# Optimization experiments

Hardware: AMD Instinct MI355X
Metric: run time of the kernel (lower is better)

Reference implementation:

```python
import jax, jax.numpy as jnp
import numpy as np


def setup_inputs() -> dict:
    key = jax.random.key(0)
    ks = jax.random.split(key, 10)
    N, CZ, CH = 512, 128, 128
    s = 1.0 / np.sqrt(CZ)  # keep pre-sigmoid activations in a sane range
    return {
        "z": jax.random.normal(ks[0], (N, N, CZ), dtype=jnp.float32),
        "mask": jnp.ones((N, N, 1), dtype=jnp.float32),
        "weight_ag": jax.random.normal(ks[1], (CH, CZ), dtype=jnp.float32) * s,
        "bias_ag": jax.random.normal(ks[2], (CH,), dtype=jnp.float32) * 0.02,
        "weight_ap": jax.random.normal(ks[3], (CH, CZ), dtype=jnp.float32) * s,
        "bias_ap": jax.random.normal(ks[4], (CH,), dtype=jnp.float32) * 0.02,
        "weight_bg": jax.random.normal(ks[5], (CH, CZ), dtype=jnp.float32) * s,
        "bias_bg": jax.random.normal(ks[6], (CH,), dtype=jnp.float32) * 0.02,
        "weight_bp": jax.random.normal(ks[7], (CH, CZ), dtype=jnp.float32) * s,
        "bias_bp": jax.random.normal(ks[8], (CH,), dtype=jnp.float32) * 0.02,
        "chunk_size": 32,
    }


def _triangle_mul(z, mask, w_ag, b_ag, w_ap, b_ap, w_bg, b_bg, w_bp, b_bp):
    # z: [N, N, c_z]; mask: [N, N, 1]; weights: [c, c_z]
    # a = mask * sigmoid(Linear_ag(z)) * Linear_ap(z)   -> [N, N, c]
    a = mask * jax.nn.sigmoid(jnp.einsum("ijz,cz->ijc", z, w_ag) + b_ag) * (
        jnp.einsum("ijz,cz->ijc", z, w_ap) + b_ap
    )
    b = mask * jax.nn.sigmoid(jnp.einsum("ijz,cz->ijc", z, w_bg) + b_bg) * (
        jnp.einsum("ijz,cz->ijc", z, w_bp) + b_bp
    )
    # outgoing triangle multiplicative combination, channel-first output [c, N, N]
    return jnp.einsum("ikc,jkc->cij", a, b)


def reference(z, mask, weight_ag, bias_ag, weight_ap, bias_ap,
              weight_bg, bias_bg, weight_bp, bias_bp, chunk_size):
    # The torch wrapper chunks the hidden-channel dim of the weights and
    # concatenates the per-chunk [c, N, N] outputs along dim 0. Since every
    # channel is independent, this is mathematically identical to running the
    # full computation at once; we do that (clean, fused form).
    return _triangle_mul(z, mask, weight_ag, bias_ag, weight_ap, bias_ap,
                         weight_bg, bias_bg, weight_bp, bias_bp)
```

## Files before the change

### kernel.cpp

```cpp
#include <hip/hip_runtime.h>
#include <stdint.h>


#define NDIM 512
#define CZ   128
#define CH   128
#define NPOS (NDIM * NDIM)

typedef __attribute__((ext_vector_type(8))) __bf16 bf16x8;
typedef __attribute__((ext_vector_type(4))) float  f32x4;

__device__ __forceinline__ unsigned short f2bf(float f) {
  unsigned int u = __builtin_bit_cast(unsigned int, f);
  unsigned int r = (u + 0x7fffu + ((u >> 16) & 1u)) >> 16;
  return (unsigned short)r;
}
__device__ __forceinline__ float bf2f_lo(unsigned int u) {
  return __builtin_bit_cast(float, u << 16);
}
__device__ __forceinline__ float bf2f_hi(unsigned int u) {
  return __builtin_bit_cast(float, u & 0xffff0000u);
}

__global__ __launch_bounds__(256) void conv_weights(
    const float* __restrict__ wag, const float* __restrict__ wap,
    const float* __restrict__ wbg, const float* __restrict__ wbp,
    unsigned short* __restrict__ wbf) {
  int idx = blockIdx.x * 256 + threadIdx.x;
  int proj = idx >> 14;
  int rem  = idx & 16383;
  const float* src = (proj == 0) ? wag : (proj == 1) ? wap : (proj == 2) ? wbg : wbp;
  wbf[idx] = f2bf(src[rem]);
}

__global__ __launch_bounds__(256, 3) void proj_fuse(
    const float* __restrict__ z,
    const float* __restrict__ mask,
    const unsigned short* __restrict__ wbf,
    const float* __restrict__ bias_ag, const float* __restrict__ bias_ap,
    const float* __restrict__ bias_bg, const float* __restrict__ bias_bp,
    unsigned short* __restrict__ a_ws,
    unsigned short* __restrict__ b_ws) {
  __shared__ unsigned short zbuf[32 * 136];
  __shared__ unsigned short accb[4 * 128 * 36];

  const int t    = threadIdx.x;
  const int lane = t & 63;
  const int w    = t >> 6;
  const int m0   = blockIdx.x * 32;

  {
    const int c4 = t & 31;
    const int rb = t >> 5;
#pragma unroll
    for (int it = 0; it < 4; ++it) {
      const int row = it * 8 + rb;
      const float4 v = *(const float4*)(z + (size_t)(m0 + row) * CZ + c4 * 4);
      unsigned int lo = (unsigned int)f2bf(v.x) | ((unsigned int)f2bf(v.y) << 16);
      unsigned int hi = (unsigned int)f2bf(v.z) | ((unsigned int)f2bf(v.w) << 16);
      *(uint2*)&zbuf[row * 136 + c4 * 4] = make_uint2(lo, hi);
    }
  }
  __syncthreads();

  const int ml    = lane & 15;
  const int q     = lane >> 4;
  const int koffl = q * 8;

  f32x4 acc[2][8];
#pragma unroll
  for (int mi = 0; mi < 2; ++mi)
#pragma unroll
    for (int ni = 0; ni < 8; ++ni) acc[mi][ni] = (f32x4){0.f, 0.f, 0.f, 0.f};

#pragma unroll
  for (int ks = 0; ks < 4; ++ks) {
    bf16x8 af0 = *(const bf16x8*)&zbuf[(ml)      * 136 + ks * 32 + koffl];
    bf16x8 af1 = *(const bf16x8*)&zbuf[(ml + 16) * 136 + ks * 32 + koffl];
#pragma unroll
    for (int ni = 0; ni < 8; ++ni) {
      bf16x8 wf = *(const bf16x8*)&wbf[((size_t)w * CH + ni * 16 + ml) * CZ + ks * 32 + koffl];
      acc[0][ni] = __builtin_amdgcn_mfma_f32_16x16x32_bf16(af0, wf, acc[0][ni], 0, 0, 0);
      acc[1][ni] = __builtin_amdgcn_mfma_f32_16x16x32_bf16(af1, wf, acc[1][ni], 0, 0, 0);
    }
  }

#pragma unroll
  for (int mi = 0; mi < 2; ++mi)
#pragma unroll
    for (int ni = 0; ni < 8; ++ni) {
      const int c    = ni * 16 + ml;
      const int pos0 = mi * 16 + q * 4;
      unsigned int lo = (unsigned int)f2bf(acc[mi][ni][0]) |
                        ((unsigned int)f2bf(acc[mi][ni][1]) << 16);
      unsigned int hi = (unsigned int)f2bf(acc[mi][ni][2]) |
                        ((unsigned int)f2bf(acc[mi][ni][3]) << 16);
      *(uint2*)&accb[((size_t)w * CH + c) * 36 + pos0] = make_uint2(lo, hi);
    }
  __syncthreads();

  const int pc = t & 7;
  const int cb = t >> 3;
  const float4 mv = *(const float4*)(mask + m0 + pc * 4);

#pragma unroll
  for (int pair = 0; pair < 2; ++pair) {
    const float* bgp = pair ? bias_bg : bias_ag;
    const float* bpp = pair ? bias_bp : bias_ap;
    unsigned short* plane = pair ? b_ws : a_ws;
    const int pg = pair * 2, pp = pg + 1;
#pragma unroll
    for (int it = 0; it < 4; ++it) {
      const int ch = it * 32 + cb;
      uint2 gv = *(const uint2*)&accb[((size_t)pg * CH + ch) * 36 + pc * 4];
      uint2 pv = *(const uint2*)&accb[((size_t)pp * CH + ch) * 36 + pc * 4];
      const float bg = bgp[ch];
      const float bp = bpp[ch];
      float g[4] = {bf2f_lo(gv.x) + bg, bf2f_hi(gv.x) + bg,
                    bf2f_lo(gv.y) + bg, bf2f_hi(gv.y) + bg};
      float p[4] = {bf2f_lo(pv.x) + bp, bf2f_hi(pv.x) + bp,
                    bf2f_lo(pv.y) + bp, bf2f_hi(pv.y) + bp};
      const float mr[4] = {mv.x, mv.y, mv.z, mv.w};
      unsigned short h[4];
#pragma unroll
      for (int r = 0; r < 4; ++r) {
        float s = 1.0f / (1.0f + __expf(-g[r]));
        h[r] = f2bf(mr[r] * s * p[r]);
      }
      *(uint2*)(plane + (size_t)ch * NPOS + m0 + pc * 4) =
          make_uint2((unsigned int)h[0] | ((unsigned int)h[1] << 16),
                     (unsigned int)h[2] | ((unsigned int)h[3] << 16));
    }
  }
}

__global__ __launch_bounds__(256, 3) void tri_gemm(
    const unsigned short* __restrict__ a_ws,
    const unsigned short* __restrict__ b_ws,
    float* __restrict__ out) {
  __shared__ unsigned short sA[128 * 64];
  __shared__ unsigned short sB[128 * 64];

  const int t = threadIdx.x, lane = t & 63, wave = t >> 6;
  const int wm = wave >> 1, wn = wave & 1;
  const int tj = blockIdx.x, ti = blockIdx.y, c = blockIdx.z;
  const int i0 = ti * 128, j0 = tj * 128;

  const unsigned short* Ap = a_ws + (size_t)c * NPOS + (size_t)i0 * NDIM;
  const unsigned short* Bp = b_ws + (size_t)c * NPOS + (size_t)j0 * NDIM;

  f32x4 acc[4][4];
#pragma unroll
  for (int mi = 0; mi < 4; ++mi)
#pragma unroll
    for (int ni = 0; ni < 4; ++ni) acc[mi][ni] = (f32x4){0.f, 0.f, 0.f, 0.f};

  const int srow8  = t >> 3;
  const int schunk = t & 7;
  const int mrow = wm * 64 + (lane & 15);
  const int nrow = wn * 64 + (lane & 15);

  for (int kk = 0; kk < 8; ++kk) {
    const int k0 = kk * 64;
#pragma unroll
    for (int i = 0; i < 4; ++i) {
      const int row = i * 32 + srow8;
      const int kcs = schunk ^ (row & 7);
      __builtin_amdgcn_global_load_lds(
          (const __attribute__((address_space(1))) unsigned int*)(Ap + (size_t)row * NDIM + k0 + kcs * 8),
          (__attribute__((address_space(3))) unsigned int*)&sA[(i * 256 + t) * 8], 16, 0, 0);
      __builtin_amdgcn_global_load_lds(
          (const __attribute__((address_space(1))) unsigned int*)(Bp + (size_t)row * NDIM + k0 + kcs * 8),
          (__attribute__((address_space(3))) unsigned int*)&sB[(i * 256 + t) * 8], 16, 0, 0);
    }
    __syncthreads();

#pragma unroll
    for (int ksub = 0; ksub < 2; ++ksub) {
      const int kc = ksub * 4 + (lane >> 4);
      bf16x8 af[4], bfr[4];
#pragma unroll
      for (int mi = 0; mi < 4; ++mi) {
        const int r = mrow + mi * 16;
        af[mi] = *(const bf16x8*)&sA[r * 64 + ((kc ^ (r & 7)) << 3)];
      }
#pragma unroll
      for (int ni = 0; ni < 4; ++ni) {
        const int r = nrow + ni * 16;
        bfr[ni] = *(const bf16x8*)&sB[r * 64 + ((kc ^ (r & 7)) << 3)];
      }
#pragma unroll
      for (int mi = 0; mi < 4; ++mi)
#pragma unroll
        for (int ni = 0; ni < 4; ++ni)
          acc[mi][ni] = __builtin_amdgcn_mfma_f32_16x16x32_bf16(af[mi], bfr[ni], acc[mi][ni], 0, 0, 0);
    }
    __syncthreads();
  }

  float* O = out + (size_t)c * NPOS + (size_t)i0 * NDIM + j0;
#pragma unroll
  for (int mi = 0; mi < 4; ++mi)
#pragma unroll
    for (int r = 0; r < 4; ++r) {
      const int m = wm * 64 + mi * 16 + (lane >> 4) * 4 + r;
#pragma unroll
      for (int ni = 0; ni < 4; ++ni) {
        const int n = wn * 64 + ni * 16 + (lane & 15);
        O[(size_t)m * NDIM + n] = acc[mi][ni][r];
      }
    }
}

extern "C" void kernel_launch(void* const* d_in, const int* in_sizes, int n_in,
                              void* d_out, int out_size, void* d_ws, size_t ws_size,
                              hipStream_t stream) {
  const float* z    = (const float*)d_in[0];
  const float* mask = (const float*)d_in[1];
  const float* wag  = (const float*)d_in[2];
  const float* bag  = (const float*)d_in[3];
  const float* wap  = (const float*)d_in[4];
  const float* bap  = (const float*)d_in[5];
  const float* wbg  = (const float*)d_in[6];
  const float* bbg  = (const float*)d_in[7];
  const float* wbp  = (const float*)d_in[8];
  const float* bbp  = (const float*)d_in[9];
  float* out = (float*)d_out;

  unsigned short* wbf  = (unsigned short*)d_ws;
  unsigned short* a_ws = (unsigned short*)((char*)d_ws + 131072);
  unsigned short* b_ws = (unsigned short*)((char*)d_ws + 131072 + (size_t)CH * NPOS * 2);

  conv_weights<<<dim3(256), dim3(256), 0, stream>>>(wag, wap, wbg, wbp, wbf);
  proj_fuse<<<dim3(NPOS / 32), dim3(256), 0, stream>>>(
      z, mask, wbf, bag, bap, bbg, bbp, a_ws, b_ws);
  tri_gemm<<<dim3(4, 4, CH), dim3(256), 0, stream>>>(a_ws, b_ws, out);
}
```

Measured before the change: 442.3 us.

## Make projection kernel persistent with register-resident weights; XCD-aware tri_gemm block mapping

```diff
diff --git a/kernel.cpp b/kernel.cpp
--- a/kernel.cpp
+++ b/kernel.cpp
@@ -6,6 +6,8 @@
 #define CZ   128
 #define CH   128
 #define NPOS (NDIM * NDIM)
+#define NTILE 16
+#define POSB  (NTILE * 32)
 
 typedef __attribute__((ext_vector_type(8))) __bf16 bf16x8;
 typedef __attribute__((ext_vector_type(4))) float  f32x4;
@@ -33,7 +35,7 @@
   wbf[idx] = f2bf(src[rem]);
 }
 
-__global__ __launch_bounds__(256, 3) void proj_fuse(
+__global__ __launch_bounds__(512, 4) void proj_fuse(
     const float* __restrict__ z,
     const float* __restrict__ mask,
     const unsigned short* __restrict__ wbf,
@@ -47,90 +49,110 @@
   const int t    = threadIdx.x;
   const int lane = t & 63;
   const int w    = t >> 6;
-  const int m0   = blockIdx.x * 32;
-
-  {
-    const int c4 = t & 31;
-    const int rb = t >> 5;
-#pragma unroll
-    for (int it = 0; it < 4; ++it) {
-      const int row = it * 8 + rb;
+  const int proj = w & 3;
+  const int half = w >> 2;
+  const int base = blockIdx.x * POSB;
+
+  const int ml    = lane & 15;
+  const int q     = lane >> 4;
+  const int koffl = q * 8;
+
+  bf16x8 wfrag[4][4];
+#pragma unroll
+  for (int ks = 0; ks < 4; ++ks)
+#pragma unroll
+    for (int ni = 0; ni < 4; ++ni)
+      wfrag[ks][ni] = *(const bf16x8*)&wbf[((size_t)proj * CH + half * 64 + ni * 16 + ml) * CZ + ks * 32 + koffl];
+
+  const int pc = t & 7;
+  const int cb = t >> 3;
+  float bga[2], bpa[2], bgb[2], bpb[2];
+#pragma unroll
+  for (int it = 0; it < 2; ++it) {
+    bga[it] = bias_ag[it * 64 + cb];
+    bpa[it] = bias_ap[it * 64 + cb];
+    bgb[it] = bias_bg[it * 64 + cb];
+    bpb[it] = bias_bp[it * 64 + cb];
+  }
+
+#pragma unroll 1
+  for (int tt = 0; tt < NTILE; ++tt) {
+    const int m0 = base + tt * 32;
+
+#pragma unroll
+    for (int it = 0; it < 2; ++it) {
+      const int id  = it * 512 + t;
+      const int row = id >> 5;
+      const int c4  = id & 31;
       const float4 v = *(const float4*)(z + (size_t)(m0 + row) * CZ + c4 * 4);
       unsigned int lo = (unsigned int)f2bf(v.x) | ((unsigned int)f2bf(v.y) << 16);
       unsigned int hi = (unsigned int)f2bf(v.z) | ((unsigned int)f2bf(v.w) << 16);
       *(uint2*)&zbuf[row * 136 + c4 * 4] = make_uint2(lo, hi);
     }
-  }
-  __syncthreads();
-
-  const int ml    = lane & 15;
-  const int q     = lane >> 4;
-  const int koffl = q * 8;
-
-  f32x4 acc[2][8];
-#pragma unroll
-  for (int mi = 0; mi < 2; ++mi)
-#pragma unroll
-    for (int ni = 0; ni < 8; ++ni) acc[mi][ni] = (f32x4){0.f, 0.f, 0.f, 0.f};
-
-#pragma unroll
-  for (int ks = 0; ks < 4; ++ks) {
-    bf16x8 af0 = *(const bf16x8*)&zbuf[(ml)      * 136 + ks * 32 + koffl];
-    bf16x8 af1 = *(const bf16x8*)&zbuf[(ml + 16) * 136 + ks * 32 + koffl];
-#pragma unroll
-    for (int ni = 0; ni < 8; ++ni) {
-      bf16x8 wf = *(const bf16x8*)&wbf[((size_t)w * CH + ni * 16 + ml) * CZ + ks * 32 + koffl];
-      acc[0][ni] = __builtin_amdgcn_mfma_f32_16x16x32_bf16(af0, wf, acc[0][ni], 0, 0, 0);
-      acc[1][ni] = __builtin_amdgcn_mfma_f32_16x16x32_bf16(af1, wf, acc[1][ni], 0, 0, 0);
-    }
-  }
-
-#pragma unroll
-  for (int mi = 0; mi < 2; ++mi)
-#pragma unroll
-    for (int ni = 0; ni < 8; ++ni) {
-      const int c    = ni * 16 + ml;
-      const int pos0 = mi * 16 + q * 4;
-      unsigned int lo = (unsigned int)f2bf(acc[mi][ni][0]) |
-                        ((unsigned int)f2bf(acc[mi][ni][1]) << 16);
-      unsigned int hi = (unsigned int)f2bf(acc[mi][ni][2]) |
-                        ((unsigned int)f2bf(acc[mi][ni][3]) << 16);
-      *(uint2*)&accb[((size_t)w * CH + c) * 36 + pos0] = make_uint2(lo, hi);
-    }
-  __syncthreads();
-
-  const int pc = t & 7;
-  const int cb = t >> 3;
-  const float4 mv = *(const float4*)(mask + m0 + pc * 4);
-
-#pragma unroll
-  for (int pair = 0; pair < 2; ++pair) {
-    const float* bgp = pair ? bias_bg : bias_ag;
-    const float* bpp = pair ? bias_bp : bias_ap;
-    unsigned short* plane = pair ? b_ws : a_ws;
-    const int pg = pair * 2, pp = pg + 1;
-#pragma unroll
-    for (int it = 0; it < 4; ++it) {
-      const int ch = it * 32 + cb;
-      uint2 gv = *(const uint2*)&accb[((size_t)pg * CH + ch) * 36 + pc * 4];
-      uint2 pv = *(const uint2*)&accb[((size_t)pp * CH + ch) * 36 + pc * 4];
-      const float bg = bgp[ch];
-      const float bp = bpp[ch];
-      float g[4] = {bf2f_lo(gv.x) + bg, bf2f_hi(gv.x) + bg,
-                    bf2f_lo(gv.y) + bg, bf2f_hi(gv.y) + bg};
-      float p[4] = {bf2f_lo(pv.x) + bp, bf2f_hi(pv.x) + bp,
-                    bf2f_lo(pv.y) + bp, bf2f_hi(pv.y) + bp};
-      const float mr[4] = {mv.x, mv.y, mv.z, mv.w};
-      unsigned short h[4];
-#pragma unroll
-      for (int r = 0; r < 4; ++r) {
-        float s = 1.0f / (1.0f + __expf(-g[r]));
-        h[r] = f2bf(mr[r] * s * p[r]);
-      }
-      *(uint2*)(plane + (size_t)ch * NPOS + m0 + pc * 4) =
-          make_uint2((unsigned int)h[0] | ((unsigned int)h[1] << 16),
-                     (unsigned int)h[2] | ((unsigned int)h[3] << 16));
-    }
+    __syncthreads();
+
+    f32x4 acc[2][4];
+#pragma unroll
+    for (int mi = 0; mi < 2; ++mi)
+#pragma unroll
+      for (int ni = 0; ni < 4; ++ni) acc[mi][ni] = (f32x4){0.f, 0.f, 0.f, 0.f};
+
+#pragma unroll
+    for (int ks = 0; ks < 4; ++ks) {
+      bf16x8 af0 = *(const bf16x8*)&zbuf[(ml)      * 136 + ks * 32 + koffl];
+      bf16x8 af1 = *(const bf16x8*)&zbuf[(ml + 16) * 136 + ks * 32 + koffl];
+#pragma unroll
+      for (int ni = 0; ni < 4; ++ni) {
+        acc[0][ni] = __builtin_amdgcn_mfma_f32_16x16x32_bf16(af0, wfrag[ks][ni], acc[0][ni], 0, 0, 0);
+        acc[1][ni] = __builtin_amdgcn_mfma_f32_16x16x32_bf16(af1, wfrag[ks][ni], acc[1][ni], 0, 0, 0);
+      }
+    }
+
+#pragma unroll
+    for (int mi = 0; mi < 2; ++mi)
+#pragma unroll
+      for (int ni = 0; ni < 4; ++ni) {
+        const int c    = half * 64 + ni * 16 + ml;
+        const int pos0 = mi * 16 + q * 4;
+        unsigned int lo = (unsigned int)f2bf(acc[mi][ni][0]) |
+                          ((unsigned int)f2bf(acc[mi][ni][1]) << 16);
+        unsigned int hi = (unsigned int)f2bf(acc[mi][ni][2]) |
+                          ((unsigned int)f2bf(acc[mi][ni][3]) << 16);
+        *(uint2*)&accb[((size_t)proj * CH + c) * 36 + pos0] = make_uint2(lo, hi);
+      }
+    __syncthreads();
+
+    const float4 mv = *(const float4*)(mask + m0 + pc * 4);
+    const float mr[4] = {mv.x, mv.y, mv.z, mv.w};
+#pragma unroll
+    for (int pair = 0; pair < 2; ++pair) {
+      const float* bgp = pair ? bgb : bga;
+      const float* bpp = pair ? bpb : bpa;
+      unsigned short* plane = pair ? b_ws : a_ws;
+      const int pg = pair * 2, pp = pg + 1;
+#pragma unroll
+      for (int it = 0; it < 2; ++it) {
+        const int ch = it * 64 + cb;
+        uint2 gv = *(const uint2*)&accb[((size_t)pg * CH + ch) * 36 + pc * 4];
+        uint2 pv = *(const uint2*)&accb[((size_t)pp * CH + ch) * 36 + pc * 4];
+        const float bg = bgp[it];
+        const float bp = bpp[it];
+        float g[4] = {bf2f_lo(gv.x) + bg, bf2f_hi(gv.x) + bg,
+                      bf2f_lo(gv.y) + bg, bf2f_hi(gv.y) + bg};
+        float p[4] = {bf2f_lo(pv.x) + bp, bf2f_hi(pv.x) + bp,
+                      bf2f_lo(pv.y) + bp, bf2f_hi(pv.y) + bp};
+        unsigned short h[4];
+#pragma unroll
+        for (int r = 0; r < 4; ++r) {
+          float s = 1.0f / (1.0f + __expf(-g[r]));
+          h[r] = f2bf(mr[r] * s * p[r]);
+        }
+        *(uint2*)(plane + (size_t)ch * NPOS + m0 + pc * 4) =
+            make_uint2((unsigned int)h[0] | ((unsigned int)h[1] << 16),
+                       (unsigned int)h[2] | ((unsigned int)h[3] << 16));
+      }
+    }
+    __syncthreads();
   }
 }
 
@@ -143,7 +165,13 @@
 
   const int t = threadIdx.x, lane = t & 63, wave = t >> 6;
   const int wm = wave >> 1, wn = wave & 1;
-  const int tj = blockIdx.x, ti = blockIdx.y, c = blockIdx.z;
+
+  const int L    = blockIdx.x;
+  const int xcd  = L & 7;
+  const int slot = L >> 3;
+  const int c    = xcd * 16 + (slot >> 4);
+  const int tile = slot & 15;
+  const int ti   = tile >> 2, tj = tile & 3;
   const int i0 = ti * 128, j0 = tj * 128;
 
   const unsigned short* Ap = a_ws + (size_t)c * NPOS + (size_t)i0 * NDIM;
@@ -232,7 +260,7 @@
   unsigned short* b_ws = (unsigned short*)((char*)d_ws + 131072 + (size_t)CH * NPOS * 2);
 
   conv_weights<<<dim3(256), dim3(256), 0, stream>>>(wag, wap, wbg, wbp, wbf);
-  proj_fuse<<<dim3(NPOS / 32), dim3(256), 0, stream>>>(
+  proj_fuse<<<dim3(NPOS / POSB), dim3(512), 0, stream>>>(
       z, mask, wbf, bag, bap, bbg, bbp, a_ws, b_ws);
-  tri_gemm<<<dim3(4, 4, CH), dim3(256), 0, stream>>>(a_ws, b_ws, out);
-}
+  tri_gemm<<<dim3(2048), dim3(256), 0, stream>>>(a_ws, b_ws, out);
+}
```

New measurement: 388.2 us. 12.2% less time.
